# Performance work log

Hardware: AMD Instinct MI355X
Metric: run time of the kernel (lower is better)

## Reference

```python
import jax, jax.numpy as jnp
import numpy as np

B, C, H, W = 2, 64, 64, 64
C2 = C // 2
N = H * W


def conv1x1(x, w, b):
    # x: (B,Cin,H,W), w: (Cout,Cin), b: (Cout,)
    return jnp.einsum('bchw,oc->bohw', x, w) + b[None, :, None, None]


def setup_inputs() -> dict:
    key = jax.random.key(0)
    ks = jax.random.split(key, 20)
    s = 0.05
    d = {
        'x1': jax.random.normal(ks[0], (B, C, H, W), jnp.float32),
        'x2': jax.random.normal(ks[1], (B, C, H, W), jnp.float32),
        'wq1': jax.random.normal(ks[2], (C2, C), jnp.float32) * s,
        'bq1': jax.random.normal(ks[3], (C2,), jnp.float32) * s,
        'wk1': jax.random.normal(ks[4], (C2, C), jnp.float32) * s,
        'bk1': jax.random.normal(ks[5], (C2,), jnp.float32) * s,
        'wv1': jax.random.normal(ks[6], (C2, C), jnp.float32) * s,
        'bv1': jax.random.normal(ks[7], (C2,), jnp.float32) * s,
        'wc1': jax.random.normal(ks[8], (C, C2), jnp.float32) * s,
        'bc1': jax.random.normal(ks[9], (C,), jnp.float32) * s,
        'wq2': jax.random.normal(ks[10], (C2, C), jnp.float32) * s,
        'bq2': jax.random.normal(ks[11], (C2,), jnp.float32) * s,
        'wk2': jax.random.normal(ks[12], (C2, C), jnp.float32) * s,
        'bk2': jax.random.normal(ks[13], (C2,), jnp.float32) * s,
        'wv2': jax.random.normal(ks[14], (C2, C), jnp.float32) * s,
        'bv2': jax.random.normal(ks[15], (C2,), jnp.float32) * s,
        'wc2': jax.random.normal(ks[16], (C, C2), jnp.float32) * s,
        'bc2': jax.random.normal(ks[17], (C,), jnp.float32) * s,
        'gamma1': jax.random.normal(ks[18], (1,), jnp.float32) * 0.5,
        'gamma2': jax.random.normal(ks[19], (1,), jnp.float32) * 0.5,
    }
    return d


def reference(x1, x2, wq1, bq1, wk1, bk1, wv1, bv1, wc1, bc1,
              wq2, bq2, wk2, bk2, wv2, bv2, wc2, bc2, gamma1, gamma2):
    b, c, h, w = x1.shape
    n = h * w
    # branch-1 projections (boundary semantics)
    q1 = jnp.max(conv1x1(x1, wq1, bq1), axis=1).reshape(b, n)          # (B,N) channel-max
    k1 = jnp.max(conv1x1(x1, wk1, bk1).reshape(b, -1, n), axis=1)      # (B,N)
    v1 = conv1x1(x1, wv1, bv1).reshape(b, -1, n)                        # (B,C/2,N)
    # branch-2 projections (field semantics)
    q2 = jnp.mean(conv1x1(x2, wq2, bq2), axis=1).reshape(b, n)         # (B,N) channel-mean
    k2 = jnp.mean(conv1x1(x2, wk2, bk2).reshape(b, -1, n), axis=1)     # (B,N)
    v2 = conv1x1(x2, wv2, bv2).reshape(b, -1, n)                        # (B,C/2,N)
    # energy2 = q1 (B,N,1) @ k2 (B,1,N) outer product; inverted sigmoid gate
    att2 = 1.0 - jax.nn.sigmoid(q1[:, :, None] * k2[:, None, :])        # (B,N,N)
    out1 = jnp.einsum('bck,bmk->bcm', v1, att2).reshape(b, c // 2, h, w)
    out1 = conv1x1(out1, wc2, bc2)
    # energy1 = q2 outer k1; sigmoid gate
    att1 = jax.nn.sigmoid(q2[:, :, None] * k1[:, None, :])              # (B,N,N)
    out2 = jnp.einsum('bck,bmk->bcm', v2, att1).reshape(b, c // 2, h, w)
    out2 = conv1x1(out2, wc1, bc1)
    out1 = x1 + gamma1[0] * out1
    out2 = x2 + gamma2[0] * out2
    return (out1, out2)
```

## Files before the change

### kernel.cpp

```cpp
#include <hip/hip_runtime.h>
#include <hip/hip_bf16.h>

#define NN 4096
#define CC 64
#define C2 32
#define BB 2

#define NSEG   4
#define M_BLK  64
#define KBLK   64
#define KB_ITERS (NN / NSEG / KBLK)

#define WS_Q1 0
#define WS_K1 8192
#define WS_Q2 16384
#define WS_K2 24576
#define WS_V1 32768
#define WS_V2 163840
#define WS_P  294912

typedef __attribute__((address_space(1))) const unsigned int GUI;
typedef __attribute__((address_space(3))) unsigned int LUI;
typedef __attribute__((ext_vector_type(8))) short bf16x8;
typedef __attribute__((ext_vector_type(4))) float f32x4;

__device__ __forceinline__ void glds16(const void* g, void* l) {
    __builtin_amdgcn_global_load_lds((GUI*)g, (LUI*)l, 16, 0, 0);
}

__device__ __forceinline__ unsigned short bf16_rne(float f) {
    union { float f; unsigned u; } x; x.f = f;
    unsigned u = x.u + 0x7fff + ((x.u >> 16) & 1);
    return (unsigned short)(u >> 16);
}
__device__ __forceinline__ unsigned pack2(float a, float b) {
    __hip_bfloat162 h = __float22bfloat162_rn(make_float2(a, b));
    unsigned r; __builtin_memcpy(&r, &h, 4); return r;
}
__device__ __forceinline__ float sigm_e2(float x) {
    return __builtin_amdgcn_rcpf(1.0f + __builtin_amdgcn_exp2f(x));
}

__global__ __launch_bounds__(256) void proj_kernel(
    const float* __restrict__ x1, const float* __restrict__ x2,
    const float* __restrict__ wq1, const float* __restrict__ bq1,
    const float* __restrict__ wk1, const float* __restrict__ bk1,
    const float* __restrict__ wv1, const float* __restrict__ bv1,
    const float* __restrict__ wq2, const float* __restrict__ bq2,
    const float* __restrict__ wk2, const float* __restrict__ bk2,
    const float* __restrict__ wv2, const float* __restrict__ bv2,
    float* __restrict__ ws)
{
    const int ln = threadIdx.x & 63;
    const int og = threadIdx.x >> 6;
    const int n  = blockIdx.x * 64 + ln;
    const int p  = blockIdx.y;
    const int b  = blockIdx.z;

    const float* x; const float* w; const float* bias;
    int mode; float* dstf; unsigned short* dstv;
    switch (p) {
      case 0: x = x1; w = wq1; bias = bq1; mode = 0; dstf = ws + WS_Q1; dstv = 0; break;
      case 1: x = x1; w = wk1; bias = bk1; mode = 0; dstf = ws + WS_K1; dstv = 0; break;
      case 2: x = x1; w = wv1; bias = bv1; mode = 2; dstf = 0; dstv = (unsigned short*)(ws + WS_V1); break;
      case 3: x = x2; w = wq2; bias = bq2; mode = 1; dstf = ws + WS_Q2; dstv = 0; break;
      case 4: x = x2; w = wk2; bias = bk2; mode = 1; dstf = ws + WS_K2; dstv = 0; break;
      default:x = x2; w = wv2; bias = bv2; mode = 2; dstf = 0; dstv = (unsigned short*)(ws + WS_V2); break;
    }

    __shared__ float red[4][C2][64];

    float acc[C2];
    #pragma unroll
    for (int o = 0; o < C2; ++o) acc[o] = 0.0f;

    const float* xb = x + ((size_t)b * CC + og * 16) * NN + n;
    #pragma unroll
    for (int ci = 0; ci < 16; ++ci) {
        const float xv = xb[(size_t)ci * NN];
        #pragma unroll
        for (int o = 0; o < C2; ++o)
            acc[o] += w[o * CC + og * 16 + ci] * xv;
    }
    #pragma unroll
    for (int o = 0; o < C2; ++o) red[og][o][ln] = acc[o];
    __syncthreads();

    float f[8];
    #pragma unroll
    for (int j = 0; j < 8; ++j) {
        const int o = og * 8 + j;
        f[j] = red[0][o][ln] + red[1][o][ln] + red[2][o][ln] + red[3][o][ln]
             + bias[o];
    }

    if (mode == 2) {
        #pragma unroll
        for (int j = 0; j < 8; ++j)
            dstv[((size_t)b * C2 + og * 8 + j) * NN + n] = bf16_rne(f[j]);
    } else {
        float r;
        if (mode == 0) {
            r = f[0];
            #pragma unroll
            for (int j = 1; j < 8; ++j) r = fmaxf(r, f[j]);
        } else {
            r = 0.0f;
            #pragma unroll
            for (int j = 0; j < 8; ++j) r += f[j];
        }
        __syncthreads();
        red[og][0][ln] = r;
        __syncthreads();
        if (og == 0) {
            const float a0 = red[0][0][ln], a1 = red[1][0][ln];
            const float a2 = red[2][0][ln], a3 = red[3][0][ln];
            const float rr = (mode == 0)
                ? fmaxf(fmaxf(a0, a1), fmaxf(a2, a3))
                : (a0 + a1 + a2 + a3) * (1.0f / C2);
            dstf[(size_t)b * NN + n] = rr;
        }
    }
}

__global__ __launch_bounds__(256) void attn_mfma(
    const float* __restrict__ q1, const float* __restrict__ k1,
    const float* __restrict__ q2, const float* __restrict__ k2,
    const unsigned short* __restrict__ v1, const unsigned short* __restrict__ v2,
    float* __restrict__ pout)
{
    __shared__ unsigned short vtile[C2 * KBLK];
    __shared__ unsigned short stile[M_BLK * KBLK];

    const int tid = threadIdx.x;
    const int wv  = tid >> 6;
    const int ln  = tid & 63;

    const int seg    = blockIdx.y;
    const int z      = blockIdx.z;
    const int branch = z & 1;
    const int b      = z >> 1;
    const int m0     = blockIdx.x * M_BLK;
    const int kstart = seg * (NN / NSEG);

    const float* q; const float* kv; const unsigned short* vbf; float sl2e;
    if (branch == 0) { q = q1; kv = k2; vbf = v1; sl2e =  1.44269504089f; }
    else             { q = q2; kv = k1; vbf = v2; sl2e = -1.44269504089f; }

    const float qs = q[(size_t)b * NN + m0 + ln] * sl2e;

    f32x4 acc[4];
    #pragma unroll
    for (int mt = 0; mt < 4; ++mt) acc[mt] = (f32x4){0.f, 0.f, 0.f, 0.f};

    const int vc = tid >> 3;
    const int vs = tid & 7;
    const unsigned short* vsrc0 = vbf + (size_t)(b * C2 + vc) * NN
                                + ((vs ^ (vc & 7)) << 3);

    for (int kb = 0; kb < KB_ITERS; ++kb) {
        const int k0 = kstart + kb * KBLK;

        glds16(vsrc0 + k0, (char*)vtile + tid * 16);

        const float* kvp = kv + (size_t)b * NN + k0 + (wv << 4);
        const float4 ka = *(const float4*)(kvp);
        const float4 kb4 = *(const float4*)(kvp + 4);
        const float4 kc = *(const float4*)(kvp + 8);
        const float4 kd = *(const float4*)(kvp + 12);

        float s[16];
        s[0]  = sigm_e2(qs * ka.x);  s[1]  = sigm_e2(qs * ka.y);
        s[2]  = sigm_e2(qs * ka.z);  s[3]  = sigm_e2(qs * ka.w);
        s[4]  = sigm_e2(qs * kb4.x); s[5]  = sigm_e2(qs * kb4.y);
        s[6]  = sigm_e2(qs * kb4.z); s[7]  = sigm_e2(qs * kb4.w);
        s[8]  = sigm_e2(qs * kc.x);  s[9]  = sigm_e2(qs * kc.y);
        s[10] = sigm_e2(qs * kc.z);  s[11] = sigm_e2(qs * kc.w);
        s[12] = sigm_e2(qs * kd.x);  s[13] = sigm_e2(qs * kd.y);
        s[14] = sigm_e2(qs * kd.z);  s[15] = sigm_e2(qs * kd.w);

        uint4 w0, w1;
        w0.x = pack2(s[0],  s[1]);  w0.y = pack2(s[2],  s[3]);
        w0.z = pack2(s[4],  s[5]);  w0.w = pack2(s[6],  s[7]);
        w1.x = pack2(s[8],  s[9]);  w1.y = pack2(s[10], s[11]);
        w1.z = pack2(s[12], s[13]); w1.w = pack2(s[14], s[15]);

        char* srow = (char*)stile + ln * 128;
        *(uint4*)(srow + ((((wv << 1) | 0) ^ (ln & 7)) << 4)) = w0;
        *(uint4*)(srow + ((((wv << 1) | 1) ^ (ln & 7)) << 4)) = w1;

        asm volatile("s_waitcnt vmcnt(0)" ::: "memory");
        __syncthreads();

        const int ct  = wv & 1;
        const int ks  = wv >> 1;
        const int col = (ks << 2) + (ln >> 4);
        const int ac  = ct * 16 + (ln & 15);
        const bf16x8 af = *(const bf16x8*)((const char*)vtile
                          + ac * 128 + ((col ^ (ac & 7)) << 4));
        #pragma unroll
        for (int mt = 0; mt < 4; ++mt) {
            const int bm = mt * 16 + (ln & 15);
            const bf16x8 bfr = *(const bf16x8*)((const char*)stile
                               + bm * 128 + ((col ^ (bm & 7)) << 4));
            acc[mt] = __builtin_amdgcn_mfma_f32_16x16x32_bf16(af, bfr, acc[mt], 0, 0, 0);
        }
        __syncthreads();
    }

    float* red = (float*)stile;
    if (wv >= 2) {
        #pragma unroll
        for (int mt = 0; mt < 4; ++mt)
            *(f32x4*)&red[((wv - 2) * 4 + mt) * 256 + ln * 4] = acc[mt];
    }
    __syncthreads();
    if (wv < 2) {
        const size_t obase = (((size_t)(branch * NSEG + seg) * BB + b) * C2) * NN;
        #pragma unroll
        for (int mt = 0; mt < 4; ++mt) {
            const f32x4 o = *(const f32x4*)&red[(wv * 4 + mt) * 256 + ln * 4];
            acc[mt].x += o.x; acc[mt].y += o.y; acc[mt].z += o.z; acc[mt].w += o.w;
            #pragma unroll
            for (int j = 0; j < 4; ++j) {
                const int c = wv * 16 + (ln >> 4) * 4 + j;
                const int m = m0 + mt * 16 + (ln & 15);
                pout[obase + (size_t)c * NN + m] = acc[mt][j];
            }
        }
    }
}

__global__ __launch_bounds__(256) void conv_kernel(
    const float* __restrict__ x1, const float* __restrict__ x2,
    const float* __restrict__ wc1, const float* __restrict__ bc1,
    const float* __restrict__ wc2, const float* __restrict__ bc2,
    const float* __restrict__ g1,  const float* __restrict__ g2,
    const float* __restrict__ p,   float* __restrict__ out)
{
    const int m      = blockIdx.x * 256 + threadIdx.x;
    const int co0    = blockIdx.y * 8;
    const int b      = blockIdx.z >> 1;
    const int branch = blockIdx.z & 1;

    const float* w; const float* bias; const float* x; float gamma; float* o;
    if (branch == 0) { w = wc2; bias = bc2; x = x1; gamma = g1[0]; o = out; }
    else             { w = wc1; bias = bc1; x = x2; gamma = g2[0]; o = out + (size_t)BB * CC * NN; }

    float s[C2];
    #pragma unroll
    for (int c = 0; c < C2; ++c) s[c] = 0.0f;

    #pragma unroll 1
    for (int seg = 0; seg < NSEG; ++seg) {
        const float* sb = p + (((size_t)(branch * NSEG + seg) * BB + b) * C2) * NN + m;
        #pragma unroll
        for (int c = 0; c < C2; ++c)
            s[c] += sb[(size_t)c * NN];
    }

    #pragma unroll
    for (int co = co0; co < co0 + 8; ++co) {
        float a = bias[co];
        #pragma unroll
        for (int c = 0; c < C2; ++c)
            a += w[co * C2 + c] * s[c];
        const size_t idx = ((size_t)b * CC + co) * NN + m;
        o[idx] = x[idx] + gamma * a;
    }
}

extern "C" void kernel_launch(void* const* d_in, const int* in_sizes, int n_in,
                              void* d_out, int out_size, void* d_ws, size_t ws_size,
                              hipStream_t stream)
{
    const float* x1  = (const float*)d_in[0];
    const float* x2  = (const float*)d_in[1];
    const float* wq1 = (const float*)d_in[2];
    const float* bq1 = (const float*)d_in[3];
    const float* wk1 = (const float*)d_in[4];
    const float* bk1 = (const float*)d_in[5];
    const float* wv1 = (const float*)d_in[6];
    const float* bv1 = (const float*)d_in[7];
    const float* wc1 = (const float*)d_in[8];
    const float* bc1 = (const float*)d_in[9];
    const float* wq2 = (const float*)d_in[10];
    const float* bq2 = (const float*)d_in[11];
    const float* wk2 = (const float*)d_in[12];
    const float* bk2 = (const float*)d_in[13];
    const float* wv2 = (const float*)d_in[14];
    const float* bv2 = (const float*)d_in[15];
    const float* wc2 = (const float*)d_in[16];
    const float* bc2 = (const float*)d_in[17];
    const float* g1  = (const float*)d_in[18];
    const float* g2  = (const float*)d_in[19];

    float* ws  = (float*)d_ws;
    float* out = (float*)d_out;

    proj_kernel<<<dim3(NN / 64, 6, BB), 256, 0, stream>>>(
        x1, x2, wq1, bq1, wk1, bk1, wv1, bv1,
        wq2, bq2, wk2, bk2, wv2, bv2, ws);

    const float* q1 = ws + WS_Q1; const float* k1 = ws + WS_K1;
    const float* q2 = ws + WS_Q2; const float* k2 = ws + WS_K2;
    const unsigned short* v1 = (const unsigned short*)(ws + WS_V1);
    const unsigned short* v2 = (const unsigned short*)(ws + WS_V2);
    float* pp = ws + WS_P;

    attn_mfma<<<dim3(NN / M_BLK, NSEG, BB * 2), 256, 0, stream>>>(
        q1, k1, q2, k2, v1, v2, pp);

    conv_kernel<<<dim3(NN / 256, 8, BB * 2), 256, 0, stream>>>(
        x1, x2, wc1, bc1, wc2, bc2, g1, g2, pp, out);
}
```

Before: 52.45 us.

## Use single-wave attention blocks with register-resident sigmoid tiles and more K segments

The attention kernel is restructured so each 64-thread block (one wave) handles 16 query rows across all 32 value channels. The sigmoid gate values are built directly into MFMA operand registers instead of being staged through an LDS tile, which removes the block-wide barriers and the cross-wave reduction. The number of K segments doubles to keep enough blocks in flight. In exchange, each V tile is loaded by four times as many blocks, and the partial-output buffer that the conv kernel must read and sum doubles in size.

New measurement: 55.08 us. 5.0% more time.

```diff
diff --git a/kernel.cpp b/kernel.cpp
--- a/kernel.cpp
+++ b/kernel.cpp
@@ -6,8 +6,8 @@
 #define C2 32
 #define BB 2
 
-#define NSEG   4
-#define M_BLK  64
+#define NSEG   8
+#define M_BLK  16
 #define KBLK   64
 #define KB_ITERS (NN / NSEG / KBLK)
 
@@ -123,19 +123,15 @@
     }
 }
 
-__global__ __launch_bounds__(256) void attn_mfma(
+__global__ __launch_bounds__(64) void attn_mfma(
     const float* __restrict__ q1, const float* __restrict__ k1,
     const float* __restrict__ q2, const float* __restrict__ k2,
     const unsigned short* __restrict__ v1, const unsigned short* __restrict__ v2,
     float* __restrict__ pout)
 {
     __shared__ unsigned short vtile[C2 * KBLK];
-    __shared__ unsigned short stile[M_BLK * KBLK];
-
-    const int tid = threadIdx.x;
-    const int wv  = tid >> 6;
-    const int ln  = tid & 63;
-
+
+    const int l = threadIdx.x;
     const int seg    = blockIdx.y;
     const int z      = blockIdx.z;
     const int branch = z & 1;
@@ -147,87 +143,70 @@
     if (branch == 0) { q = q1; kv = k2; vbf = v1; sl2e =  1.44269504089f; }
     else             { q = q2; kv = k1; vbf = v2; sl2e = -1.44269504089f; }
 
-    const float qs = q[(size_t)b * NN + m0 + ln] * sl2e;
-
-    f32x4 acc[4];
-    #pragma unroll
-    for (int mt = 0; mt < 4; ++mt) acc[mt] = (f32x4){0.f, 0.f, 0.f, 0.f};
-
-    const int vc = tid >> 3;
-    const int vs = tid & 7;
-    const unsigned short* vsrc0 = vbf + (size_t)(b * C2 + vc) * NN
-                                + ((vs ^ (vc & 7)) << 3);
-
-    for (int kb = 0; kb < KB_ITERS; ++kb) {
-        const int k0 = kstart + kb * KBLK;
-
-        glds16(vsrc0 + k0, (char*)vtile + tid * 16);
-
-        const float* kvp = kv + (size_t)b * NN + k0 + (wv << 4);
-        const float4 ka = *(const float4*)(kvp);
-        const float4 kb4 = *(const float4*)(kvp + 4);
-        const float4 kc = *(const float4*)(kvp + 8);
-        const float4 kd = *(const float4*)(kvp + 12);
-
-        float s[16];
-        s[0]  = sigm_e2(qs * ka.x);  s[1]  = sigm_e2(qs * ka.y);
-        s[2]  = sigm_e2(qs * ka.z);  s[3]  = sigm_e2(qs * ka.w);
-        s[4]  = sigm_e2(qs * kb4.x); s[5]  = sigm_e2(qs * kb4.y);
-        s[6]  = sigm_e2(qs * kb4.z); s[7]  = sigm_e2(qs * kb4.w);
-        s[8]  = sigm_e2(qs * kc.x);  s[9]  = sigm_e2(qs * kc.y);
-        s[10] = sigm_e2(qs * kc.z);  s[11] = sigm_e2(qs * kc.w);
-        s[12] = sigm_e2(qs * kd.x);  s[13] = sigm_e2(qs * kd.y);
-        s[14] = sigm_e2(qs * kd.z);  s[15] = sigm_e2(qs * kd.w);
+    const int m16 = l & 15;
+    const int kq  = l >> 4;
+    const float qs = q[(size_t)b * NN + m0 + m16] * sl2e;
+    const float* kvb = kv + (size_t)b * NN;
+
+    const int vr = l >> 3;
+    const int vs = l & 7;
+    const unsigned short* vsrc = vbf + ((size_t)b * C2 + vr) * NN
+                               + ((vs ^ vr) << 3);
+
+    f32x4 acc0 = (f32x4){0.f, 0.f, 0.f, 0.f};
+    f32x4 acc1 = (f32x4){0.f, 0.f, 0.f, 0.f};
+
+    for (int t = 0; t < KB_ITERS; ++t) {
+        const int k0 = kstart + t * KBLK;
+
+        asm volatile("s_waitcnt lgkmcnt(0)" ::: "memory");
+
+        const float4 ka0 = *(const float4*)(kvb + k0 + kq * 8);
+        const float4 kb0 = *(const float4*)(kvb + k0 + kq * 8 + 4);
+        const float4 ka1 = *(const float4*)(kvb + k0 + 32 + kq * 8);
+        const float4 kb1 = *(const float4*)(kvb + k0 + 32 + kq * 8 + 4);
+
+        #pragma unroll
+        for (int j = 0; j < 4; ++j)
+            glds16(vsrc + (size_t)j * 8 * NN + k0,
+                   (char*)vtile + j * 1024 + l * 16);
 
         uint4 w0, w1;
-        w0.x = pack2(s[0],  s[1]);  w0.y = pack2(s[2],  s[3]);
-        w0.z = pack2(s[4],  s[5]);  w0.w = pack2(s[6],  s[7]);
-        w1.x = pack2(s[8],  s[9]);  w1.y = pack2(s[10], s[11]);
-        w1.z = pack2(s[12], s[13]); w1.w = pack2(s[14], s[15]);
-
-        char* srow = (char*)stile + ln * 128;
-        *(uint4*)(srow + ((((wv << 1) | 0) ^ (ln & 7)) << 4)) = w0;
-        *(uint4*)(srow + ((((wv << 1) | 1) ^ (ln & 7)) << 4)) = w1;
+        w0.x = pack2(sigm_e2(qs * ka0.x), sigm_e2(qs * ka0.y));
+        w0.y = pack2(sigm_e2(qs * ka0.z), sigm_e2(qs * ka0.w));
+        w0.z = pack2(sigm_e2(qs * kb0.x), sigm_e2(qs * kb0.y));
+        w0.w = pack2(sigm_e2(qs * kb0.z), sigm_e2(qs * kb0.w));
+        w1.x = pack2(sigm_e2(qs * ka1.x), sigm_e2(qs * ka1.y));
+        w1.y = pack2(sigm_e2(qs * ka1.z), sigm_e2(qs * ka1.w));
+        w1.z = pack2(sigm_e2(qs * kb1.x), sigm_e2(qs * kb1.y));
+        w1.w = pack2(sigm_e2(qs * kb1.z), sigm_e2(qs * kb1.w));
+        bf16x8 bf0, bf1;
+        __builtin_memcpy(&bf0, &w0, 16);
+        __builtin_memcpy(&bf1, &w1, 16);
 
         asm volatile("s_waitcnt vmcnt(0)" ::: "memory");
-        __syncthreads();
-
-        const int ct  = wv & 1;
-        const int ks  = wv >> 1;
-        const int col = (ks << 2) + (ln >> 4);
-        const int ac  = ct * 16 + (ln & 15);
-        const bf16x8 af = *(const bf16x8*)((const char*)vtile
-                          + ac * 128 + ((col ^ (ac & 7)) << 4));
-        #pragma unroll
-        for (int mt = 0; mt < 4; ++mt) {
-            const int bm = mt * 16 + (ln & 15);
-            const bf16x8 bfr = *(const bf16x8*)((const char*)stile
-                               + bm * 128 + ((col ^ (bm & 7)) << 4));
-            acc[mt] = __builtin_amdgcn_mfma_f32_16x16x32_bf16(af, bfr, acc[mt], 0, 0, 0);
+        __builtin_amdgcn_sched_barrier(0);
+
+        #pragma unroll
+        for (int kh = 0; kh < 2; ++kh) {
+            const int slot = kh * 4 + kq;
+            const int r0 = m16;
+            const int r1 = 16 + m16;
+            const bf16x8 a0 = *(const bf16x8*)((const char*)vtile
+                              + r0 * 128 + ((slot ^ (r0 & 7)) << 4));
+            const bf16x8 a1 = *(const bf16x8*)((const char*)vtile
+                              + r1 * 128 + ((slot ^ (r1 & 7)) << 4));
+            const bf16x8 bfr = kh ? bf1 : bf0;
+            acc0 = __builtin_amdgcn_mfma_f32_16x16x32_bf16(a0, bfr, acc0, 0, 0, 0);
+            acc1 = __builtin_amdgcn_mfma_f32_16x16x32_bf16(a1, bfr, acc1, 0, 0, 0);
         }
-        __syncthreads();
-    }
-
-    float* red = (float*)stile;
-    if (wv >= 2) {
-        #pragma unroll
-        for (int mt = 0; mt < 4; ++mt)
-            *(f32x4*)&red[((wv - 2) * 4 + mt) * 256 + ln * 4] = acc[mt];
-    }
-    __syncthreads();
-    if (wv < 2) {
-        const size_t obase = (((size_t)(branch * NSEG + seg) * BB + b) * C2) * NN;
-        #pragma unroll
-        for (int mt = 0; mt < 4; ++mt) {
-            const f32x4 o = *(const f32x4*)&red[(wv * 4 + mt) * 256 + ln * 4];
-            acc[mt].x += o.x; acc[mt].y += o.y; acc[mt].z += o.z; acc[mt].w += o.w;
-            #pragma unroll
-            for (int j = 0; j < 4; ++j) {
-                const int c = wv * 16 + (ln >> 4) * 4 + j;
-                const int m = m0 + mt * 16 + (ln & 15);
-                pout[obase + (size_t)c * NN + m] = acc[mt][j];
-            }
-        }
+    }
+
+    const size_t obase = (((size_t)(branch * NSEG + seg) * BB + b) * C2) * NN;
+    #pragma unroll
+    for (int j = 0; j < 4; ++j) {
+        pout[obase + (size_t)(kq * 4 + j) * NN + m0 + m16]      = acc0[j];
+        pout[obase + (size_t)(16 + kq * 4 + j) * NN + m0 + m16] = acc1[j];
     }
 }
 
@@ -308,9 +287,9 @@
     const unsigned short* v2 = (const unsigned short*)(ws + WS_V2);
     float* pp = ws + WS_P;
 
-    attn_mfma<<<dim3(NN / M_BLK, NSEG, BB * 2), 256, 0, stream>>>(
+    attn_mfma<<<dim3(NN / M_BLK, NSEG, BB * 2), 64, 0, stream>>>(
         q1, k1, q2, k2, v1, v2, pp);
 
-    conv_kernel<<<dim3(NN / 256, 8, BB * 2), 256, 0, stream>>>(
+    conv_kernel<<<dim3(NN / 256, NSEG, BB * 2), 256, 0, stream>>>(
         x1, x2, wc1, bc1, wc2, bc2, g1, g2, pp, out);
 }
```
